# Performance work log

Measured on AMD Instinct MI355X. Metric: run time of the kernel, lower is better.

Reference implementation:

```python
import jax, jax.numpy as jnp
import numpy as np

NUM_FIELDS = 40
EMBED_DIM = 64
ATTN_DIM = 32

def _triu_index(n):
    i, j = np.triu_indices(n, k=1)
    return jnp.asarray(i, jnp.int32), jnp.asarray(j, jnp.int32)

def setup_inputs() -> dict:
    key = jax.random.key(0)
    k0, k1, k2, k3, k4, k5 = jax.random.split(key, 6)
    B = 8192
    inputs = jax.random.normal(k0, (B, NUM_FIELDS, EMBED_DIM), dtype=jnp.float32)
    # attention MLP params (PyTorch Linear default init scale ~ 1/sqrt(fan_in))
    s1 = 1.0 / np.sqrt(EMBED_DIM)
    s2 = 1.0 / np.sqrt(ATTN_DIM)
    W1 = jax.random.uniform(k1, (EMBED_DIM, ATTN_DIM), jnp.float32, -s1, s1)
    b1 = jax.random.uniform(k2, (ATTN_DIM,), jnp.float32, -s1, s1)
    w2 = jax.random.uniform(k3, (ATTN_DIM,), jnp.float32, -s2, s2)
    p = jax.random.uniform(k4, (EMBED_DIM,), jnp.float32, -s1, s1)
    return {"inputs": inputs, "W1": W1, "b1": b1, "w2": w2, "p": p}

def reference(inputs, W1, b1, w2, p):
    idx0, idx1 = _triu_index(NUM_FIELDS)  # [P], P = 780 pairs
    # gather pairwise field embeddings and take elementwise product: [B, P, D]
    prod = inputs[:, idx0, :] * inputs[:, idx1, :]
    # tiny attention MLP: Linear -> ReLU -> Linear(no bias) -> softmax over pairs
    h = jax.nn.relu(jnp.einsum('bpd,da->bpa', prod, W1) + b1)  # [B, P, A]
    logits = jnp.einsum('bpa,a->bp', h, w2)                    # [B, P]
    attn = jax.nn.softmax(logits, axis=1)                      # softmax over pair dim
    # attention-weighted sum pooling over pairs: [B, D]
    pooled = jnp.einsum('bp,bpd->bd', attn, prod)
    # final linear projection to scalar (dropout=0 / eval -> identity)
    return jnp.einsum('bd,d->b', pooled, p)
```

## Files before the change

kernel.cpp:

```cpp
#include <hip/hip_runtime.h>


typedef _Float16 f16;
typedef f16 f16x2 __attribute__((ext_vector_type(2)));
typedef f16 f16x4 __attribute__((ext_vector_type(4)));
typedef f16 f16x8 __attribute__((ext_vector_type(8)));
typedef float fx16 __attribute__((ext_vector_type(16)));

#define NF 40
#define NB 8192
#define STR 76

union V8 { f16x8 v8; f16x4 v4[2]; f16x2 v2[4]; };

__global__ __launch_bounds__(256, 4) void afm_kernel(
    const float* __restrict__ x,
    const float* __restrict__ W1,
    const float* __restrict__ b1,
    const float* __restrict__ w2,
    const float* __restrict__ p,
    float* __restrict__ out)
{
    __shared__ f16 xh[2][NF * STR];
    __shared__ float red[2][2][2];

    const int tid  = threadIdx.x;
    const int wid  = tid >> 6;
    const int lane = tid & 63;
    const int bl   = wid >> 1;
    const int role = wid & 1;
    const int b0   = blockIdx.x * 2;

    f16* Xs = &xh[bl][0];

    const float4* xb = (const float4*)(x + (size_t)b0 * (NF * 64));
#pragma unroll
    for (int t = 0; t < 3; ++t) {
        int g = t * 256 + tid;
        if (g < 640) {
            float4 v0 = xb[g * 2];
            float4 v1 = xb[g * 2 + 1];
            f16x4 lo = { (f16)v0.x, (f16)v0.y, (f16)v0.z, (f16)v0.w };
            f16x4 hi = { (f16)v1.x, (f16)v1.y, (f16)v1.z, (f16)v1.w };
            int bsel = (g >= 320);
            int gi = g - (bsel ? 320 : 0);
            int row = gi >> 3, gg = gi & 7;
            f16* dst = &xh[bsel][0] + row * STR + gg * 8;
            *(f16x4*)dst = lo;
            *(f16x4*)(dst + 4) = hi;
        }
    }
    __syncthreads();

    const int nl = lane & 31;
    const int hh = lane >> 5;
    const int h8 = hh * 8;

    f16x8 w1f[4];
#pragma unroll
    for (int kt = 0; kt < 4; ++kt)
#pragma unroll
        for (int j = 0; j < 8; ++j)
            w1f[kt][j] = (f16)W1[(kt * 16 + h8 + j) * 32 + nl];

    f16x2 pp[16];
#pragma unroll
    for (int kt = 0; kt < 4; ++kt)
#pragma unroll
        for (int m = 0; m < 4; ++m) {
            f16x2 t2 = { (f16)p[kt * 16 + h8 + 2 * m], (f16)p[kt * 16 + h8 + 2 * m + 1] };
            pp[kt * 4 + m] = t2;
        }

    fx16 b1C;
    f16x2 w2h[8];
#pragma unroll
    for (int r = 0; r < 16; ++r) {
        int a = (r & 3) + 8 * (r >> 2) + 4 * hh;
        b1C[r] = b1[a];
    }
#pragma unroll
    for (int m = 0; m < 8; ++m) {
        int r = 2 * m;
        int a = (r & 3) + 8 * (r >> 2) + 4 * hh;
        f16x2 t2 = { (f16)(w2[a] * 1.44269504f), (f16)(w2[a + 1] * 1.44269504f) };
        w2h[m] = t2;
    }

    f16x4 xif[8];
    {
        const f16* src = Xs + nl * STR + h8;
#pragma unroll
        for (int kt = 0; kt < 4; ++kt) {
            xif[2 * kt]     = *(const f16x4*)(src + kt * 16);
            xif[2 * kt + 1] = *(const f16x4*)(src + kt * 16 + 4);
        }
    }

    float accW = 0.f, accWS = 0.f;

    auto body = [&](const f16x4* xi, int jrow, bool valid) {
        const f16* base = Xs + jrow * STR + h8;
        V8 pr[4];
#pragma unroll
        for (int kt = 0; kt < 4; ++kt) {
            f16x4 a0 = *(const f16x4*)(base + kt * 16);
            f16x4 a1 = *(const f16x4*)(base + kt * 16 + 4);
            pr[kt].v4[0] = xi[2 * kt] * a0;
            pr[kt].v4[1] = xi[2 * kt + 1] * a1;
        }
        fx16 C = __builtin_amdgcn_mfma_f32_32x32x16_f16(w1f[0], pr[0].v8, b1C, 0, 0, 0);
        C = __builtin_amdgcn_mfma_f32_32x32x16_f16(w1f[1], pr[1].v8, C, 0, 0, 0);
        C = __builtin_amdgcn_mfma_f32_32x32x16_f16(w1f[2], pr[2].v8, C, 0, 0, 0);
        C = __builtin_amdgcn_mfma_f32_32x32x16_f16(w1f[3], pr[3].v8, C, 0, 0, 0);
        float s0 = 0.f, s1 = 0.f, s2 = 0.f, s3 = 0.f;
#pragma unroll
        for (int m = 0; m < 4; ++m) {
            s0 = __builtin_amdgcn_fdot2(pr[0].v2[m], pp[m],      s0, false);
            s1 = __builtin_amdgcn_fdot2(pr[1].v2[m], pp[4 + m],  s1, false);
            s2 = __builtin_amdgcn_fdot2(pr[2].v2[m], pp[8 + m],  s2, false);
            s3 = __builtin_amdgcn_fdot2(pr[3].v2[m], pp[12 + m], s3, false);
        }
        float sp = (s0 + s1) + (s2 + s3);
        const f16x2 z2 = { (f16)0.f, (f16)0.f };
        float l0 = 0.f, l1 = 0.f;
#pragma unroll
        for (int m = 0; m < 8; ++m) {
            f16x2 hm = __builtin_bit_cast(f16x2,
                __builtin_amdgcn_cvt_pkrtz(C[2 * m], C[2 * m + 1]));
            hm = __builtin_elementwise_max(hm, z2);
            if (m & 1) l1 = __builtin_amdgcn_fdot2(hm, w2h[m], l1, false);
            else       l0 = __builtin_amdgcn_fdot2(hm, w2h[m], l0, false);
        }
        float l = l0 + l1;
        l  += __shfl_xor(l, 32);
        sp += __shfl_xor(sp, 32);
        float w = __builtin_amdgcn_exp2f(l);
        if (!valid) w = 0.f;
        accW += w;
        accWS = fmaf(w, sp, accWS);
    };

    const int tb = 1 + role * 12;
    for (int t = tb; t < tb + 12; ++t) {
        int jrow = (t <= 16) ? ((nl + t) & 31) : (t + 15);
        bool valid = (t != 16) || (nl < 16);
        body(xif, jrow, valid);
    }
    if (role) {
        int q = nl < 28 ? nl : 27;
        float disc = 225.0f - 8.0f * (float)q;
        int ii = (int)((15.0f - sqrtf(disc)) * 0.5f);
        if (ii * (15 - ii) / 2 > q) --ii;
        if ((ii + 1) * (14 - ii) / 2 <= q) ++ii;
        int jj = q - ii * (15 - ii) / 2 + ii + 1;
        int iC = 32 + ii, jC = 32 + jj;
        f16x4 xi2[8];
        const f16* src = Xs + iC * STR + h8;
#pragma unroll
        for (int kt = 0; kt < 4; ++kt) {
            xi2[2 * kt]     = *(const f16x4*)(src + kt * 16);
            xi2[2 * kt + 1] = *(const f16x4*)(src + kt * 16 + 4);
        }
        body(xi2, jC, nl < 28);
    }

#pragma unroll
    for (int m = 16; m >= 1; m >>= 1) {
        accW  += __shfl_xor(accW, m);
        accWS += __shfl_xor(accWS, m);
    }
    if (lane == 0) {
        red[bl][role][0] = accW;
        red[bl][role][1] = accWS;
    }
    __syncthreads();
    if (tid < 2) {
        float W = red[tid][0][0] + red[tid][1][0];
        float S = red[tid][0][1] + red[tid][1][1];
        out[b0 + tid] = S / W;
    }
}

extern "C" void kernel_launch(void* const* d_in, const int* in_sizes, int n_in,
                              void* d_out, int out_size, void* d_ws, size_t ws_size,
                              hipStream_t stream) {
    const float* x  = (const float*)d_in[0];
    const float* W1 = (const float*)d_in[1];
    const float* b1 = (const float*)d_in[2];
    const float* w2 = (const float*)d_in[3];
    const float* p  = (const float*)d_in[4];
    float* out = (float*)d_out;
    dim3 grid(NB / 2), block(256);
    hipLaunchKernelGGL(afm_kernel, grid, block, 0, stream, x, W1, b1, w2, p, out);
}
```

Before: 152.3 us.

## Assign one batch row per block with four waves splitting pair tiles

Each block now handles a single batch row instead of two. All four waves share one LDS tile and each processes 6 of the 24 pair-diagonal steps, with the last wave also handling the leftover 28 tail pairs. The grid doubles to one block per row and the final reduction combines four wave partials. This halves per-block LDS and shortens the serial per-wave loop, but leaves the tail work unbalanced on one wave and adds more per-block setup such as weight-fragment loads.

Result: slower. 178.1 us (+16.9%).

```diff
diff --git a/kernel.cpp b/kernel.cpp
--- a/kernel.cpp
+++ b/kernel.cpp
@@ -21,31 +21,25 @@
     const float* __restrict__ p,
     float* __restrict__ out)
 {
-    __shared__ f16 xh[2][NF * STR];
-    __shared__ float red[2][2][2];
+    __shared__ f16 xh[NF * STR];
+    __shared__ float red[4][2];
 
     const int tid  = threadIdx.x;
     const int wid  = tid >> 6;
     const int lane = tid & 63;
-    const int bl   = wid >> 1;
-    const int role = wid & 1;
-    const int b0   = blockIdx.x * 2;
+    const int b    = blockIdx.x;
 
-    f16* Xs = &xh[bl][0];
-
-    const float4* xb = (const float4*)(x + (size_t)b0 * (NF * 64));
+    const float4* xb = (const float4*)(x + (size_t)b * (NF * 64));
 #pragma unroll
-    for (int t = 0; t < 3; ++t) {
+    for (int t = 0; t < 2; ++t) {
         int g = t * 256 + tid;
-        if (g < 640) {
+        if (g < 320) {
             float4 v0 = xb[g * 2];
             float4 v1 = xb[g * 2 + 1];
             f16x4 lo = { (f16)v0.x, (f16)v0.y, (f16)v0.z, (f16)v0.w };
             f16x4 hi = { (f16)v1.x, (f16)v1.y, (f16)v1.z, (f16)v1.w };
-            int bsel = (g >= 320);
-            int gi = g - (bsel ? 320 : 0);
-            int row = gi >> 3, gg = gi & 7;
-            f16* dst = &xh[bsel][0] + row * STR + gg * 8;
+            int row = g >> 3, gg = g & 7;
+            f16* dst = xh + row * STR + gg * 8;
             *(f16x4*)dst = lo;
             *(f16x4*)(dst + 4) = hi;
         }
@@ -89,7 +83,7 @@
 
     f16x4 xif[8];
     {
-        const f16* src = Xs + nl * STR + h8;
+        const f16* src = xh + nl * STR + h8;
 #pragma unroll
         for (int kt = 0; kt < 4; ++kt) {
             xif[2 * kt]     = *(const f16x4*)(src + kt * 16);
@@ -100,7 +94,7 @@
     float accW = 0.f, accWS = 0.f;
 
     auto body = [&](const f16x4* xi, int jrow, bool valid) {
-        const f16* base = Xs + jrow * STR + h8;
+        const f16* base = xh + jrow * STR + h8;
         V8 pr[4];
 #pragma unroll
         for (int kt = 0; kt < 4; ++kt) {
@@ -141,13 +135,13 @@
         accWS = fmaf(w, sp, accWS);
     };
 
-    const int tb = 1 + role * 12;
-    for (int t = tb; t < tb + 12; ++t) {
+    const int tb = 1 + wid * 6;
+    for (int t = tb; t < tb + 6; ++t) {
         int jrow = (t <= 16) ? ((nl + t) & 31) : (t + 15);
         bool valid = (t != 16) || (nl < 16);
         body(xif, jrow, valid);
     }
-    if (role) {
+    if (wid == 3) {
         int q = nl < 28 ? nl : 27;
         float disc = 225.0f - 8.0f * (float)q;
         int ii = (int)((15.0f - sqrtf(disc)) * 0.5f);
@@ -156,7 +150,7 @@
         int jj = q - ii * (15 - ii) / 2 + ii + 1;
         int iC = 32 + ii, jC = 32 + jj;
         f16x4 xi2[8];
-        const f16* src = Xs + iC * STR + h8;
+        const f16* src = xh + iC * STR + h8;
 #pragma unroll
         for (int kt = 0; kt < 4; ++kt) {
             xi2[2 * kt]     = *(const f16x4*)(src + kt * 16);
@@ -171,14 +165,14 @@
         accWS += __shfl_xor(accWS, m);
     }
     if (lane == 0) {
-        red[bl][role][0] = accW;
-        red[bl][role][1] = accWS;
+        red[wid][0] = accW;
+        red[wid][1] = accWS;
     }
     __syncthreads();
-    if (tid < 2) {
-        float W = red[tid][0][0] + red[tid][1][0];
-        float S = red[tid][0][1] + red[tid][1][1];
-        out[b0 + tid] = S / W;
+    if (tid == 0) {
+        float W = (red[0][0] + red[1][0]) + (red[2][0] + red[3][0]);
+        float S = (red[0][1] + red[1][1]) + (red[2][1] + red[3][1]);
+        out[b] = S / W;
     }
 }
 
@@ -191,6 +185,6 @@
     const float* w2 = (const float*)d_in[3];
     const float* p  = (const float*)d_in[4];
     float* out = (float*)d_out;
-    dim3 grid(NB / 2), block(256);
+    dim3 grid(NB), block(256);
     hipLaunchKernelGGL(afm_kernel, grid, block, 0, stream, x, W1, b1, w2, p, out);
 }
```
